# Kernel tuning notes

Hardware: AMD Instinct MI355X
Metric: run time of the kernel (lower is better)

The kernel has to match this reference:

```python
import jax, jax.numpy as jnp
import numpy as np
import math

D_MODEL, N_HEAD, N_KV_HEAD, MAX_LEN = 2048, 32, 8, 2048
D_K = D_MODEL // N_HEAD
BASE = 10000.0
B, T = 2, 2048


def _rope_tables(seq_len):
    # matches torch Rotary: cos/sin of shape [seq_len, D_K], repeat_interleave(2) over freq dim
    inv_freq = 1.0 / (BASE ** (jnp.arange(0, D_K, 2, dtype=jnp.float32) / D_K))
    t = jnp.arange(seq_len, dtype=jnp.float32)[:, None] * inv_freq  # [T, D_K/2]
    cos = jnp.repeat(jnp.cos(t), 2, axis=-1)  # [T, D_K]
    sin = jnp.repeat(jnp.sin(t), 2, axis=-1)
    return cos, sin


def _rotate_half(x):
    # faithful to source: x1 = even lanes, x2 = odd lanes, concat([-x2, x1], -1)
    x1, x2 = x[..., ::2], x[..., 1::2]
    return jnp.concatenate([-x2, x1], axis=-1)


def _apply_rope(x, cos, sin):
    return x * cos + _rotate_half(x) * sin


def setup_inputs() -> dict:
    key = jax.random.key(0)
    ks = jax.random.split(key, 5)
    s = 1.0 / math.sqrt(D_MODEL)
    x = jax.random.normal(ks[0], (B, T, D_MODEL), dtype=jnp.float32)
    Wq = jax.random.normal(ks[1], (D_MODEL, N_HEAD * D_K), dtype=jnp.float32) * s
    Wk = jax.random.normal(ks[2], (D_MODEL, N_KV_HEAD * D_K), dtype=jnp.float32) * s
    Wv = jax.random.normal(ks[3], (D_MODEL, N_KV_HEAD * D_K), dtype=jnp.float32) * s
    Wo = jax.random.normal(ks[4], (N_HEAD * D_K, D_MODEL), dtype=jnp.float32) * s
    mask = jnp.tril(jnp.ones((T, T), dtype=bool))  # causal
    return {"x": x, "mask": mask, "Wq": Wq, "Wk": Wk, "Wv": Wv, "Wo": Wo}


def reference(x, mask, Wq, Wk, Wv, Wo):
    b, t, _ = x.shape
    g = N_HEAD // N_KV_HEAD
    q = (x @ Wq).reshape(b, t, N_HEAD, D_K).transpose(0, 2, 1, 3)      # [B,H,T,d]
    k = (x @ Wk).reshape(b, t, N_KV_HEAD, D_K).transpose(0, 2, 1, 3)   # [B,Hkv,T,d]
    v = (x @ Wv).reshape(b, t, N_KV_HEAD, D_K).transpose(0, 2, 1, 3)
    cos, sin = _rope_tables(t)
    q = _apply_rope(q, cos, sin)
    k = _apply_rope(k, cos, sin)  # rope before/after repeat is identical per-head
    # grouped attention: q head h attends kv head h // g (repeat_interleave semantics)
    qg = q.reshape(b, N_KV_HEAD, g, t, D_K)
    scores = jnp.einsum("bkgtd,bksd->bkgts", qg, k) / math.sqrt(D_K)
    neg = jnp.finfo(scores.dtype).min
    scores = jnp.where(mask[None, None, None, :, :], scores, neg)
    attn = jax.nn.softmax(scores, axis=-1)
    out = jnp.einsum("bkgts,bksd->bkgtd", attn, v)
    out = out.reshape(b, N_HEAD, t, D_K).transpose(0, 2, 1, 3).reshape(b, t, N_HEAD * D_K)
    return out @ Wo
```

## Files before the change

### kernel.cpp

```cpp
#include <hip/hip_runtime.h>
#include <cstdint>
#include <cstddef>

typedef unsigned short u16;
typedef __attribute__((ext_vector_type(8))) short bf16x8;
typedef __attribute__((ext_vector_type(8))) unsigned short u16x8;
typedef __attribute__((ext_vector_type(4))) unsigned short u16x4;
typedef __attribute__((ext_vector_type(4))) float f32x4;

__device__ __forceinline__ unsigned short f2bf(float f) {
    union { float f; uint32_t u; } c; c.f = f;
    uint32_t u = c.u + 0x7fffu + ((c.u >> 16) & 1u);
    return (unsigned short)(u >> 16);
}
__device__ __forceinline__ float bf2f(unsigned short h) {
    union { uint32_t u; float f; } c; c.u = ((uint32_t)h) << 16;
    return c.f;
}
__device__ __forceinline__ uint32_t cvtpk(float a, float b) {
    uint32_t r;
    asm("v_cvt_pk_bf16_f32 %0, %1, %2" : "=v"(r) : "v"(a), "v"(b));
    return r;
}

#define GLDS16(g, l)                                                               \
    __builtin_amdgcn_global_load_lds((const __attribute__((address_space(1))) void*)(g), \
                                     (__attribute__((address_space(3))) void*)(l), 16, 0, 0)

__global__ __launch_bounds__(256) void cvt_x(const float* __restrict__ src,
                                             u16* __restrict__ dst) {
    int i = blockIdx.x * 256 + threadIdx.x;
    const float4* s = (const float4*)src + (size_t)i * 2;
    float4 a = s[0], b = s[1];
    u16x8 o;
    o[0] = f2bf(a.x); o[1] = f2bf(a.y); o[2] = f2bf(a.z); o[3] = f2bf(a.w);
    o[4] = f2bf(b.x); o[5] = f2bf(b.y); o[6] = f2bf(b.z); o[7] = f2bf(b.w);
    *(u16x8*)(dst + (size_t)i * 8) = o;
}

__global__ __launch_bounds__(256) void tcvt(const float* __restrict__ src,
                                            u16* __restrict__ dst, int C) {
    __shared__ u16 tile[32][33];
    const int t = threadIdx.x;
    const int bx = blockIdx.x, by = blockIdx.y;
    const int tr = t >> 3, tc = (t & 7) << 2;
    float4 f = *(const float4*)&src[(size_t)(by * 32 + tr) * C + bx * 32 + tc];
    tile[tr][tc + 0] = f2bf(f.x); tile[tr][tc + 1] = f2bf(f.y);
    tile[tr][tc + 2] = f2bf(f.z); tile[tr][tc + 3] = f2bf(f.w);
    __syncthreads();
    u16x4 o;
    o[0] = tile[tc + 0][tr]; o[1] = tile[tc + 1][tr];
    o[2] = tile[tc + 2][tr]; o[3] = tile[tc + 3][tr];
    *(u16x4*)&dst[(size_t)(bx * 32 + tr) * 2048 + by * 32 + tc] = o;
}

__global__ __launch_bounds__(256) void tcvt3(const float* __restrict__ Wq,
                                             const float* __restrict__ Wk,
                                             const float* __restrict__ Wv,
                                             u16* __restrict__ dst) {
    __shared__ u16 tile[32][33];
    const int t = threadIdx.x;
    const int bxg = blockIdx.x, by = blockIdx.y;
    const float* src; int C, nb; u16* dbase;
    if (bxg < 64)      { src = Wq; C = 2048; nb = bxg;      dbase = dst; }
    else if (bxg < 80) { src = Wk; C = 512;  nb = bxg - 64; dbase = dst + (size_t)2048 * 2048; }
    else               { src = Wv; C = 512;  nb = bxg - 80; dbase = dst + (size_t)2560 * 2048; }
    const int tr = t >> 3, tc = (t & 7) << 2;
    float4 f = *(const float4*)&src[(size_t)(by * 32 + tr) * C + nb * 32 + tc];
    tile[tr][tc + 0] = f2bf(f.x); tile[tr][tc + 1] = f2bf(f.y);
    tile[tr][tc + 2] = f2bf(f.z); tile[tr][tc + 3] = f2bf(f.w);
    __syncthreads();
    u16x4 o;
    o[0] = tile[tc + 0][tr]; o[1] = tile[tc + 1][tr];
    o[2] = tile[tc + 2][tr]; o[3] = tile[tc + 3][tr];
    *(u16x4*)&dbase[(size_t)(nb * 32 + tr) * 2048 + by * 32 + tc] = o;
}

template <int MODE>
__global__ __launch_bounds__(256) void gemm2(const u16* __restrict__ A,
                                             const u16* __restrict__ Bt,
                                             u16* __restrict__ oq, u16* __restrict__ ok,
                                             u16* __restrict__ ov, float* __restrict__ of) {
    __shared__ u16 As[128 * 32];
    __shared__ u16 Bs[128 * 32];
    const int t = threadIdx.x, w = t >> 6, lane = t & 63;
    const int l15 = lane & 15, quad = lane >> 4;
    const int m0 = blockIdx.y << 7, n0 = blockIdx.x << 7;
    const int K = 2048;
    const int c0 = w * 2, c1 = c0 + 1;
    const int ar0 = c0 * 16 + (lane >> 2), ar1 = c1 * 16 + (lane >> 2);
    const int ac = (lane & 3) << 3;
    const u16* Ap0 = A + (size_t)(m0 + ar0) * K + ac;
    const u16* Ap1 = A + (size_t)(m0 + ar1) * K + ac;
    const u16* Bp0 = Bt + (size_t)(n0 + ar0) * K + ac;
    const u16* Bp1 = Bt + (size_t)(n0 + ar1) * K + ac;
    const int wm = (w >> 1) << 6, wn = (w & 1) << 6;

    f32x4 acc[4][4] = {};

    for (int k0 = 0; k0 < K; k0 += 32) {
        GLDS16(Ap0 + k0, &As[c0 * 512]);
        GLDS16(Ap1 + k0, &As[c1 * 512]);
        GLDS16(Bp0 + k0, &Bs[c0 * 512]);
        GLDS16(Bp1 + k0, &Bs[c1 * 512]);
        __syncthreads();
        bf16x8 a[4], bfr[4];
#pragma unroll
        for (int mt = 0; mt < 4; ++mt)
            a[mt] = *(bf16x8*)&As[(wm + mt * 16 + l15) * 32 + quad * 8];
#pragma unroll
        for (int nt = 0; nt < 4; ++nt)
            bfr[nt] = *(bf16x8*)&Bs[(wn + nt * 16 + l15) * 32 + quad * 8];
#pragma unroll
        for (int mt = 0; mt < 4; ++mt)
#pragma unroll
            for (int nt = 0; nt < 4; ++nt)
                acc[mt][nt] = __builtin_amdgcn_mfma_f32_16x16x32_bf16(a[mt], bfr[nt], acc[mt][nt], 0, 0, 0);
        __syncthreads();
    }

#pragma unroll
    for (int mt = 0; mt < 4; ++mt)
#pragma unroll
        for (int nt = 0; nt < 4; ++nt)
#pragma unroll
            for (int r = 0; r < 4; ++r) {
                int row = m0 + wm + mt * 16 + quad * 4 + r;
                int col = n0 + wn + nt * 16 + l15;
                of[(size_t)row * 2048 + col] = acc[mt][nt][r];
            }
}

__global__ __launch_bounds__(512, 1) void gemm8p(const u16* __restrict__ A,
                                                 const u16* __restrict__ Bt,
                                                 u16* __restrict__ oq, u16* __restrict__ ok,
                                                 u16* __restrict__ ov) {
    __shared__ u16 lds[65536];

    const int t = threadIdx.x, w = t >> 6, lane = t & 63;
    const int l15 = lane & 15, quad = lane >> 4;
    const int wm = w >> 2, wn = w & 3;
    const int m0 = blockIdx.y << 8, n0 = blockIdx.x << 8;
    const int K = 2048;
    const int NIT = 16;

    const int srow = w * 8 + (lane >> 3);
    const int scol = ((lane & 7) ^ (lane >> 3)) << 3;
    const u16* pA = A + (size_t)(m0 + srow) * K + scol;
    const u16* pB = Bt + (size_t)(n0 + srow) * K + scol;

#define STG(AB, BUF, HF, T) do {                                                   \
    const u16* _s = ((AB) ? pB : pA) + (size_t)((HF) * 128) * K + (size_t)(T) * 64; \
    u16* _d = &lds[(BUF) * 32768 + (AB) * 16384 + (HF) * 8192 + w * 512];          \
    GLDS16(_s, _d);                                                                \
    GLDS16(_s + (size_t)64 * K, _d + 4096);                                        \
} while (0)

#define RD_A(BUF, MQ)                                                              \
    _Pragma("unroll") for (int fi = 0; fi < 4; ++fi)                               \
    _Pragma("unroll") for (int ks = 0; ks < 2; ++ks) {                             \
        int r_ = (MQ) * 64 + fi * 16 + l15;                                        \
        int u_ = ks * 4 + quad;                                                    \
        a_[fi][ks] = *(const bf16x8*)&lds[(BUF) * 32768 + wm * 8192 + r_ * 64 +    \
                                          ((u_ ^ (r_ & 7)) << 3)];                 \
    }
#define RD_B(BUF, NQ)                                                              \
    _Pragma("unroll") for (int fj = 0; fj < 2; ++fj)                               \
    _Pragma("unroll") for (int ks = 0; ks < 2; ++ks) {                             \
        int r_ = (wn & 1) * 64 + (NQ) * 32 + fj * 16 + l15;                        \
        int u_ = ks * 4 + quad;                                                    \
        b_[fj][ks] = *(const bf16x8*)&lds[(BUF) * 32768 + 16384 + (wn >> 1) * 8192 \
                                          + r_ * 64 + ((u_ ^ (r_ & 7)) << 3)];     \
    }
#define MFMA16(MQ, NQ)                                                             \
    __builtin_amdgcn_s_barrier();                                                  \
    __builtin_amdgcn_s_setprio(1);                                                 \
    _Pragma("unroll") for (int fi = 0; fi < 4; ++fi)                               \
    _Pragma("unroll") for (int fj = 0; fj < 2; ++fj) {                             \
        acc[(MQ) * 4 + fi][(NQ) * 2 + fj] = __builtin_amdgcn_mfma_f32_16x16x32_bf16( \
            a_[fi][0], b_[fj][0], acc[(MQ) * 4 + fi][(NQ) * 2 + fj], 0, 0, 0);     \
        acc[(MQ) * 4 + fi][(NQ) * 2 + fj] = __builtin_amdgcn_mfma_f32_16x16x32_bf16( \
            a_[fi][1], b_[fj][1], acc[(MQ) * 4 + fi][(NQ) * 2 + fj], 0, 0, 0);     \
    }                                                                              \
    __builtin_amdgcn_s_setprio(0);

    f32x4 acc[8][4] = {};
    bf16x8 a_[4][2], b_[2][2];

    STG(0, 0, 0, 0); STG(0, 0, 1, 0);
    STG(1, 0, 0, 0); STG(1, 0, 1, 0);
    STG(1, 1, 0, 1); STG(1, 1, 1, 1);
    asm volatile("s_waitcnt vmcnt(4)" ::: "memory");
    __builtin_amdgcn_s_barrier();

    for (int it = 0; it < NIT; ++it) {
        const bool more = (it + 1 < NIT);
        const int o = 2 * it + 1, e2 = 2 * it + 2, o2 = 2 * it + 3;

        RD_A(0, 0); RD_B(0, 0);
        STG(0, 1, 0, o);
        MFMA16(0, 0);
        __builtin_amdgcn_s_barrier();

        RD_A(0, 1);
        STG(0, 1, 1, o);
        MFMA16(1, 0);
        __builtin_amdgcn_s_barrier();

        RD_A(0, 0); RD_B(0, 1);
        MFMA16(0, 1);
        __builtin_amdgcn_s_barrier();

        RD_A(0, 1);
        if (more) { STG(1, 0, 0, e2); STG(1, 0, 1, e2); }
        MFMA16(1, 1);
        if (more) asm volatile("s_waitcnt vmcnt(4)" ::: "memory");
        else      asm volatile("s_waitcnt vmcnt(0)" ::: "memory");
        __builtin_amdgcn_s_barrier();

        RD_A(1, 0); RD_B(1, 0);
        if (more) STG(0, 0, 0, e2);
        MFMA16(0, 0);
        __builtin_amdgcn_s_barrier();

        RD_A(1, 1);
        if (more) STG(0, 0, 1, e2);
        MFMA16(1, 0);
        __builtin_amdgcn_s_barrier();

        RD_A(1, 0); RD_B(1, 1);
        MFMA16(0, 1);
        __builtin_amdgcn_s_barrier();

        RD_A(1, 1);
        if (more) { STG(1, 1, 0, o2); STG(1, 1, 1, o2); }
        MFMA16(1, 1);
        if (more) asm volatile("s_waitcnt vmcnt(4)" ::: "memory");
        else      asm volatile("s_waitcnt vmcnt(0)" ::: "memory");
        __builtin_amdgcn_s_barrier();
    }
#undef STG
#undef RD_A
#undef RD_B
#undef MFMA16

    const int colbase = n0 + wn * 64;
    const bool isv = (colbase >= 2560);
    float iv[4];
    if (!isv) {
#pragma unroll
        for (int nj = 0; nj < 4; ++nj)
            iv[nj] = exp2f(-0.4152410118609253f * (float)(nj * 8 + (l15 >> 1)));
    }
    const int map1 = (quad << 4) | ((2 * l15 + 1) & 15);
    const int map2 = (quad << 4) | ((2 * l15) & 15);
    const bool lo = (l15 < 8);
#pragma unroll
    for (int mi = 0; mi < 8; ++mi)
#pragma unroll
        for (int r = 0; r < 4; ++r) {
            const int row = m0 + wm * 128 + mi * 16 + quad * 4 + r;
            float v0 = acc[mi][0][r], v1 = acc[mi][1][r];
            float v2 = acc[mi][2][r], v3 = acc[mi][3][r];
            float o0 = v0, o1 = v1, o2 = v2, o3 = v3;
            if (!isv) {
                float g1a = __shfl(v0, map1), g1b = __shfl(v1, map1);
                float g1c = __shfl(v2, map1), g1d = __shfl(v3, map1);
                float g2a = __shfl(v0, map2), g2b = __shfl(v1, map2);
                float g2c = __shfl(v2, map2), g2d = __shfl(v3, map2);
                float p0 = lo ? g1a : g1b;
                float p1 = lo ? g1c : g1d;
                float p2 = lo ? g2a : g2b;
                float p3 = lo ? g2c : g2d;
                const float tt = (float)(row & 2047);
                float sn, cs;
                __sincosf(tt * iv[0], &sn, &cs); o0 = v0 * cs - p0 * sn;
                __sincosf(tt * iv[1], &sn, &cs); o1 = v1 * cs - p1 * sn;
                __sincosf(tt * iv[2], &sn, &cs); o2 = v2 * cs + p2 * sn;
                __sincosf(tt * iv[3], &sn, &cs); o3 = v3 * cs + p3 * sn;
            }
            float oo[4] = {o0, o1, o2, o3};
            if (colbase < 2048) {
#pragma unroll
                for (int nj = 0; nj < 4; ++nj)
                    oq[(size_t)row * 2048 + colbase + nj * 16 + l15] = f2bf(oo[nj]);
            } else if (colbase < 2560) {
#pragma unroll
                for (int nj = 0; nj < 4; ++nj)
                    ok[(size_t)row * 512 + colbase - 2048 + nj * 16 + l15] = f2bf(oo[nj]);
            } else {
#pragma unroll
                for (int nj = 0; nj < 4; ++nj)
                    ov[(size_t)(colbase - 2560 + nj * 16 + l15) * 4096 + row] = f2bf(oo[nj]);
            }
        }
}

__global__ __launch_bounds__(256, 2) void attn8(const u16* __restrict__ q,
                                                const u16* __restrict__ k,
                                                const u16* __restrict__ vT,
                                                u16* __restrict__ att) {
    __shared__ u16 Ks[64 * 64];
    __shared__ u16 Vt[64 * 64];
    __shared__ u16 Pw[4][2][16 * 64];

    const int t = threadIdx.x, w = t >> 6, lane = t & 63;
    const int l15 = lane & 15, quad = lane >> 4;
    const int id = blockIdx.x;
    const int kvh = id & 7;
    const int z = (id >> 3) & 1;
    const int gi = id >> 4;
    const int p = gi & 15;
    int g;
    switch (gi >> 4) {
        case 0:  g = 63 - p; break;
        case 1:  g = 32 + p; break;
        case 2:  g = 31 - p; break;
        default: g = p;      break;
    }
    const int h = kvh * 4 + w;
    const size_t rowbase = (size_t)z * 2048;
    const float SC = 0.125f * 1.4426950408889634f;
    const int swz = l15 & 7;

    const int srow = t >> 3;
    const int slot = t & 7;
    const int sd = slot << 3;
    const int lidx = srow * 64 + ((slot ^ (srow & 7)) << 3);

    const u16* kbase = &k[(rowbase + srow) * 512 + kvh * 64 + sd];
    const u16* vbase = &vT[(size_t)(kvh * 64 + srow) * 4096 + rowbase + sd];

    const int ntiles = (g >> 1) + 1;
    const int qrow0 = g * 32;

    bf16x8 aq[2][2];
#pragma unroll
    for (int m = 0; m < 2; ++m)
#pragma unroll
        for (int kc = 0; kc < 2; ++kc)
            aq[m][kc] = *(const bf16x8*)&q[(rowbase + qrow0 + m * 16 + l15) * 2048 +
                                           h * 64 + kc * 32 + quad * 8];

    f32x4 acc[2][4] = {};
    float m_i[2] = {-INFINITY, -INFINITY};
    float l_i[2] = {0.f, 0.f};

    u16x8 pk0 = *(const u16x8*)kbase;
    u16x8 pk1 = *(const u16x8*)(kbase + (size_t)32 * 512);
    u16x8 pv0 = *(const u16x8*)vbase;
    u16x8 pv1 = *(const u16x8*)(vbase + (size_t)32 * 4096);

    for (int kb = 0; kb < ntiles; ++kb) {
        __syncthreads();
        *(u16x8*)&Ks[lidx]        = pk0;
        *(u16x8*)&Ks[lidx + 2048] = pk1;
        *(u16x8*)&Vt[lidx]        = pv0;
        *(u16x8*)&Vt[lidx + 2048] = pv1;
        if (kb + 1 < ntiles) {
            const u16* kp = kbase + (size_t)(kb + 1) * 64 * 512;
            pk0 = *(const u16x8*)kp;
            pk1 = *(const u16x8*)(kp + (size_t)32 * 512);
            const u16* vp = vbase + (size_t)(kb + 1) * 64;
            pv0 = *(const u16x8*)vp;
            pv1 = *(const u16x8*)(vp + (size_t)32 * 4096);
        }
        __syncthreads();

        f32x4 st[2][4] = {};
        __builtin_amdgcn_s_setprio(1);
#pragma unroll
        for (int kt = 0; kt < 4; ++kt) {
            bf16x8 ak0 = *(const bf16x8*)&Ks[(kt * 16 + l15) * 64 + ((quad ^ swz) << 3)];
            bf16x8 ak1 = *(const bf16x8*)&Ks[(kt * 16 + l15) * 64 + (((quad + 4) ^ swz) << 3)];
#pragma unroll
            for (int m = 0; m < 2; ++m) {
                st[m][kt] = __builtin_amdgcn_mfma_f32_16x16x32_bf16(ak0, aq[m][0], st[m][kt], 0, 0, 0);
                st[m][kt] = __builtin_amdgcn_mfma_f32_16x16x32_bf16(ak1, aq[m][1], st[m][kt], 0, 0, 0);
            }
        }
        __builtin_amdgcn_s_setprio(0);

        const bool diag = (kb == ntiles - 1);
        float alpha_[2];
        bool resc[2];
#pragma unroll
        for (int m = 0; m < 2; ++m) {
            float sv[16];
#pragma unroll
            for (int kt = 0; kt < 4; ++kt)
#pragma unroll
                for (int r = 0; r < 4; ++r) sv[kt * 4 + r] = st[m][kt][r];
            if (diag) {
                const int qg = qrow0 + m * 16 + l15;
#pragma unroll
                for (int kt = 0; kt < 4; ++kt)
#pragma unroll
                    for (int r = 0; r < 4; ++r) {
                        int key = kb * 64 + kt * 16 + quad * 4 + r;
                        if (key > qg) sv[kt * 4 + r] = -INFINITY;
                    }
            }
            float mx = sv[0];
#pragma unroll
            for (int i = 1; i < 16; ++i) mx = fmaxf(mx, sv[i]);
            mx = fmaxf(mx, __shfl_xor(mx, 16));
            mx = fmaxf(mx, __shfl_xor(mx, 32));
            mx *= SC;
            const float mold = m_i[m];
            const bool need = __any(mx > mold + 8.f);
            float al = 1.f;
            if (need) {
                const float mnew = fmaxf(mold, mx);
                al = __builtin_amdgcn_exp2f(mold - mnew);
                m_i[m] = mnew;
            }
            const float mu = m_i[m];
            float sum = 0.f;
#pragma unroll
            for (int i = 0; i < 16; ++i) {
                sv[i] = __builtin_amdgcn_exp2f(fmaf(sv[i], SC, -mu));
                sum += sv[i];
            }
            sum += __shfl_xor(sum, 16);
            sum += __shfl_xor(sum, 32);
            l_i[m] = l_i[m] * al + sum;
            alpha_[m] = al;
            resc[m] = need;

            u16* Pq = &Pw[w][m][0];
#pragma unroll
            for (int kt = 0; kt < 4; ++kt) {
                uint2 uu;
                uu.x = cvtpk(sv[kt * 4 + 0], sv[kt * 4 + 1]);
                uu.y = cvtpk(sv[kt * 4 + 2], sv[kt * 4 + 3]);
                *(uint2*)&Pq[l15 * 64 + (((2 * kt + (quad >> 1)) ^ swz) << 3) + ((quad & 1) << 2)] = uu;
            }
        }

#pragma unroll
        for (int m = 0; m < 2; ++m)
            if (resc[m]) {
                const float al = alpha_[m];
#pragma unroll
                for (int dt = 0; dt < 4; ++dt)
#pragma unroll
                    for (int r = 0; r < 4; ++r) acc[m][dt][r] *= al;
            }

        bf16x8 bp[2][2];
#pragma unroll
        for (int m = 0; m < 2; ++m) {
            const u16* Pq = &Pw[w][m][0];
            bp[m][0] = *(const bf16x8*)&Pq[l15 * 64 + ((quad ^ swz) << 3)];
            bp[m][1] = *(const bf16x8*)&Pq[l15 * 64 + (((quad + 4) ^ swz) << 3)];
        }

        __builtin_amdgcn_s_setprio(1);
#pragma unroll
        for (int dt = 0; dt < 4; ++dt) {
            bf16x8 av0 = *(const bf16x8*)&Vt[(dt * 16 + l15) * 64 + ((quad ^ swz) << 3)];
            bf16x8 av1 = *(const bf16x8*)&Vt[(dt * 16 + l15) * 64 + (((quad + 4) ^ swz) << 3)];
#pragma unroll
            for (int m = 0; m < 2; ++m) {
                acc[m][dt] = __builtin_amdgcn_mfma_f32_16x16x32_bf16(av0, bp[m][0], acc[m][dt], 0, 0, 0);
                acc[m][dt] = __builtin_amdgcn_mfma_f32_16x16x32_bf16(av1, bp[m][1], acc[m][dt], 0, 0, 0);
            }
        }
        __builtin_amdgcn_s_setprio(0);
    }

#pragma unroll
    for (int m = 0; m < 2; ++m) {
        float inv = 1.0f / l_i[m];
        size_t row = rowbase + qrow0 + m * 16 + l15;
#pragma unroll
        for (int dt = 0; dt < 4; ++dt) {
            uint2 uu;
            uu.x = cvtpk(acc[m][dt][0] * inv, acc[m][dt][1] * inv);
            uu.y = cvtpk(acc[m][dt][2] * inv, acc[m][dt][3] * inv);
            *(uint2*)&att[row * 2048 + h * 64 + dt * 16 + quad * 4] = uu;
        }
    }
}

extern "C" void kernel_launch(void* const* d_in, const int* in_sizes, int n_in,
                              void* d_out, int out_size, void* d_ws, size_t ws_size,
                              hipStream_t stream) {
    const float* x  = (const float*)d_in[0];
    const float* Wq = (const float*)d_in[2];
    const float* Wk = (const float*)d_in[3];
    const float* Wv = (const float*)d_in[4];
    const float* Wo = (const float*)d_in[5];
    float* out = (float*)d_out;

    u16* xb = (u16*)d_out;

    u16* q     = (u16*)d_ws;
    u16* kk    = q + (size_t)4096 * 2048;
    u16* vt    = kk + (size_t)4096 * 512;
    u16* wqkvt = vt + (size_t)4096 * 512;
    u16* att   = wqkvt;
    u16* wot   = kk;

    cvt_x<<<4096, 256, 0, stream>>>(x, xb);
    tcvt3<<<dim3(96, 64), 256, 0, stream>>>(Wq, Wk, Wv, wqkvt);
    gemm8p<<<dim3(12, 16), 512, 0, stream>>>(xb, wqkvt, q, kk, vt);
    attn8<<<1024, 256, 0, stream>>>(q, kk, vt, att);
    tcvt<<<dim3(64, 64), 256, 0, stream>>>(Wo, wot, 2048);
    gemm2<1><<<dim3(16, 32), 256, 0, stream>>>(att, wot, nullptr, nullptr, nullptr, out);
}
```

Baseline: 328.4 us.

## Load all B fragments once per stage and sweep A in quarter-row steps

Reorganizes the inner GEMM loop of the fused QKV projection kernel so each wave loads all four B fragments once per buffer stage and then streams A in four 32-row quarters. The old order reloaded A twice and B in halves. This cuts LDS reads per stage, since A is no longer read twice. In exchange the B register footprint grows, the A footprint shrinks, and the interleaving of global loads with MFMA phases changes.

```diff
diff --git a/kernel.cpp b/kernel.cpp
--- a/kernel.cpp
+++ b/kernel.cpp
@@ -156,36 +156,36 @@
     GLDS16(_s + (size_t)64 * K, _d + 4096);                                        \
 } while (0)
 
-#define RD_A(BUF, MQ)                                                              \
-    _Pragma("unroll") for (int fi = 0; fi < 4; ++fi)                               \
+#define RD_A2(BUF, MQ)                                                             \
+    _Pragma("unroll") for (int fi = 0; fi < 2; ++fi)                               \
     _Pragma("unroll") for (int ks = 0; ks < 2; ++ks) {                             \
-        int r_ = (MQ) * 64 + fi * 16 + l15;                                        \
+        int r_ = (MQ) * 32 + fi * 16 + l15;                                        \
         int u_ = ks * 4 + quad;                                                    \
         a_[fi][ks] = *(const bf16x8*)&lds[(BUF) * 32768 + wm * 8192 + r_ * 64 +    \
                                           ((u_ ^ (r_ & 7)) << 3)];                 \
     }
-#define RD_B(BUF, NQ)                                                              \
-    _Pragma("unroll") for (int fj = 0; fj < 2; ++fj)                               \
+#define RD_B8(BUF)                                                                 \
+    _Pragma("unroll") for (int fj = 0; fj < 4; ++fj)                               \
     _Pragma("unroll") for (int ks = 0; ks < 2; ++ks) {                             \
-        int r_ = (wn & 1) * 64 + (NQ) * 32 + fj * 16 + l15;                        \
+        int r_ = (wn & 1) * 64 + fj * 16 + l15;                                    \
         int u_ = ks * 4 + quad;                                                    \
         b_[fj][ks] = *(const bf16x8*)&lds[(BUF) * 32768 + 16384 + (wn >> 1) * 8192 \
                                           + r_ * 64 + ((u_ ^ (r_ & 7)) << 3)];     \
     }
-#define MFMA16(MQ, NQ)                                                             \
+#define MFMA16Q(MQ)                                                                \
     __builtin_amdgcn_s_barrier();                                                  \
     __builtin_amdgcn_s_setprio(1);                                                 \
-    _Pragma("unroll") for (int fi = 0; fi < 4; ++fi)                               \
-    _Pragma("unroll") for (int fj = 0; fj < 2; ++fj) {                             \
-        acc[(MQ) * 4 + fi][(NQ) * 2 + fj] = __builtin_amdgcn_mfma_f32_16x16x32_bf16( \
-            a_[fi][0], b_[fj][0], acc[(MQ) * 4 + fi][(NQ) * 2 + fj], 0, 0, 0);     \
-        acc[(MQ) * 4 + fi][(NQ) * 2 + fj] = __builtin_amdgcn_mfma_f32_16x16x32_bf16( \
-            a_[fi][1], b_[fj][1], acc[(MQ) * 4 + fi][(NQ) * 2 + fj], 0, 0, 0);     \
+    _Pragma("unroll") for (int fi = 0; fi < 2; ++fi)                               \
+    _Pragma("unroll") for (int fj = 0; fj < 4; ++fj) {                             \
+        acc[(MQ) * 2 + fi][fj] = __builtin_amdgcn_mfma_f32_16x16x32_bf16(          \
+            a_[fi][0], b_[fj][0], acc[(MQ) * 2 + fi][fj], 0, 0, 0);                \
+        acc[(MQ) * 2 + fi][fj] = __builtin_amdgcn_mfma_f32_16x16x32_bf16(          \
+            a_[fi][1], b_[fj][1], acc[(MQ) * 2 + fi][fj], 0, 0, 0);                \
     }                                                                              \
     __builtin_amdgcn_s_setprio(0);
 
     f32x4 acc[8][4] = {};
-    bf16x8 a_[4][2], b_[2][2];
+    bf16x8 a_[2][2], b_[4][2];
 
     STG(0, 0, 0, 0); STG(0, 0, 1, 0);
     STG(1, 0, 0, 0); STG(1, 0, 1, 0);
@@ -197,52 +197,52 @@
         const bool more = (it + 1 < NIT);
         const int o = 2 * it + 1, e2 = 2 * it + 2, o2 = 2 * it + 3;
 
-        RD_A(0, 0); RD_B(0, 0);
+        RD_B8(0); RD_A2(0, 0);
         STG(0, 1, 0, o);
-        MFMA16(0, 0);
-        __builtin_amdgcn_s_barrier();
-
-        RD_A(0, 1);
+        MFMA16Q(0);
+        __builtin_amdgcn_s_barrier();
+
+        RD_A2(0, 1);
         STG(0, 1, 1, o);
-        MFMA16(1, 0);
-        __builtin_amdgcn_s_barrier();
-
-        RD_A(0, 0); RD_B(0, 1);
-        MFMA16(0, 1);
-        __builtin_amdgcn_s_barrier();
-
-        RD_A(0, 1);
+        MFMA16Q(1);
+        __builtin_amdgcn_s_barrier();
+
+        RD_A2(0, 2);
+        MFMA16Q(2);
+        __builtin_amdgcn_s_barrier();
+
+        RD_A2(0, 3);
         if (more) { STG(1, 0, 0, e2); STG(1, 0, 1, e2); }
-        MFMA16(1, 1);
+        MFMA16Q(3);
         if (more) asm volatile("s_waitcnt vmcnt(4)" ::: "memory");
         else      asm volatile("s_waitcnt vmcnt(0)" ::: "memory");
         __builtin_amdgcn_s_barrier();
 
-        RD_A(1, 0); RD_B(1, 0);
+        RD_B8(1); RD_A2(1, 0);
         if (more) STG(0, 0, 0, e2);
-        MFMA16(0, 0);
-        __builtin_amdgcn_s_barrier();
-
-        RD_A(1, 1);
+        MFMA16Q(0);
+        __builtin_amdgcn_s_barrier();
+
+        RD_A2(1, 1);
         if (more) STG(0, 0, 1, e2);
-        MFMA16(1, 0);
-        __builtin_amdgcn_s_barrier();
-
-        RD_A(1, 0); RD_B(1, 1);
-        MFMA16(0, 1);
-        __builtin_amdgcn_s_barrier();
-
-        RD_A(1, 1);
+        MFMA16Q(1);
+        __builtin_amdgcn_s_barrier();
+
+        RD_A2(1, 2);
+        MFMA16Q(2);
+        __builtin_amdgcn_s_barrier();
+
+        RD_A2(1, 3);
         if (more) { STG(1, 1, 0, o2); STG(1, 1, 1, o2); }
-        MFMA16(1, 1);
+        MFMA16Q(3);
         if (more) asm volatile("s_waitcnt vmcnt(4)" ::: "memory");
         else      asm volatile("s_waitcnt vmcnt(0)" ::: "memory");
         __builtin_amdgcn_s_barrier();
     }
 #undef STG
-#undef RD_A
-#undef RD_B
-#undef MFMA16
+#undef RD_A2
+#undef RD_B8
+#undef MFMA16Q
 
     const int colbase = n0 + wn * 64;
     const bool isv = (colbase >= 2560);
```

Result: no change. 325.3 us (-0.9%).
